# Optimization experiments

Measured on AMD Instinct MI355X. Metric: run time of the kernel, lower is better.

The kernel has to match this reference:

```python
import jax, jax.numpy as jnp
import numpy as np

N = 100_000      # nodes
E = 1_600_000    # edges (avg degree 16)
DIN = 128
DOUT = 128
NEG_SLOPE = 0.2  # DGL GATConv default negative_slope


def setup_inputs() -> dict:
    key = jax.random.key(0)
    k1, k2, k3, k4, k5, k6 = jax.random.split(key, 6)
    h = jax.random.normal(k1, (N, DIN), dtype=jnp.float32)
    src = jax.random.randint(k2, (E,), 0, N, dtype=jnp.int32)
    dst = jax.random.randint(k3, (E,), 0, N, dtype=jnp.int32)
    W = jax.random.normal(k4, (DIN, DOUT), dtype=jnp.float32) / np.sqrt(DIN).astype(np.float32)
    attn_l = jax.random.normal(k5, (DOUT,), dtype=jnp.float32) * 0.1
    attn_r = jax.random.normal(k6, (DOUT,), dtype=jnp.float32) * 0.1
    return {"h": h, "src": src, "dst": dst, "W": W, "attn_l": attn_l, "attn_r": attn_r}


def reference(h, src, dst, W, attn_l, attn_r):
    # Single-head DGL GATConv (bias=False, no feat/attn dropout, no activation).
    feat = h @ W                                   # [N, D] projected features
    el = feat @ attn_l                             # [N] source attention logits
    er = feat @ attn_r                             # [N] destination attention logits
    e = jax.nn.leaky_relu(el[src] + er[dst], NEG_SLOPE)   # [E] edge scores

    # Numerically stable edge softmax, grouped by destination node.
    m = jax.ops.segment_max(e, dst, num_segments=N)        # [N]
    m = jnp.where(jnp.isfinite(m), m, 0.0)                 # nodes with no in-edges
    ex = jnp.exp(e - m[dst])                               # [E]
    denom = jax.ops.segment_sum(ex, dst, num_segments=N)   # [N]
    alpha = ex / jnp.maximum(denom[dst], jnp.float32(1e-9))  # [E]

    # Weighted aggregation of source features into destination nodes.
    out = jax.ops.segment_sum(alpha[:, None] * feat[src], dst, num_segments=N)  # [N, D]
    return out
```

## Files before the change

### kernel.cpp

```cpp
#include <hip/hip_runtime.h>
#include <hip/hip_bf16.h>

#define N_NODES 100000
#define N_EDGES 1600000
#define D 128
#define NEG_SLOPE 0.2f

#define NBKT 782
#define CAPB 4096
#define BCHUNK 8192
#define BIN_BLOCKS 196
#define GEMM_BLOCKS 782
#define CAP 2816

typedef __attribute__((ext_vector_type(8))) short s8v;
typedef __attribute__((ext_vector_type(4))) float f4v;

static __device__ __forceinline__ unsigned short f2bf(float f) {
    __hip_bfloat16 b = __float2bfloat16(f);
    return *(unsigned short*)&b;
}

__global__ __launch_bounds__(256) void wcast(
    const float* __restrict__ W, const float* __restrict__ attn_l,
    const float* __restrict__ attn_r, unsigned short* __restrict__ Wt)
{
    __shared__ float Wl[128 * 132];
    __shared__ float all[128], arl[128];
    const int t = threadIdx.x;
    for (int i = 0; i < 64; ++i) {
        const int id = t + 256 * i;
        Wl[(id >> 7) * 132 + (id & 127)] = W[id];
    }
    if (t < 128) { all[t] = attn_l[t]; arl[t] = attn_r[t]; }
    __syncthreads();
    for (int i = 0; i < 64; ++i) {
        const int id = t + 256 * i;
        const int n = id >> 7, k = id & 127;
        Wt[n * 128 + k] = f2bf(Wl[k * 132 + n]);
    }
    if (t < 128) {
        float sl = 0.f, sr = 0.f;
        for (int n = 0; n < 128; ++n) {
            const float v = Wl[t * 132 + n];
            sl += v * all[n]; sr += v * arl[n];
        }
        Wt[128 * 128 + t] = f2bf(sl);
        Wt[129 * 128 + t] = f2bf(sr);
    }
}

__global__ __launch_bounds__(512) void gemm_bin(
    const float* __restrict__ h, const unsigned short* __restrict__ Wt,
    unsigned short* __restrict__ featb, float* __restrict__ el, float* __restrict__ er,
    const int* __restrict__ src, const int* __restrict__ dst,
    int* __restrict__ gwp, unsigned int* __restrict__ eb)
{
    __shared__ __align__(16) char smem[69632];
    const int t = threadIdx.x;

    if (blockIdx.x < BIN_BLOCKS) {
        int* cnt_l            = (int*)smem;
        int* tmp              = (int*)(smem + 3128);
        int* lbase            = (int*)(smem + 7224);
        int* gbase            = (int*)(smem + 10356);
        unsigned int* slocal  = (unsigned int*)(smem + 13484);
        unsigned short* sbkt  = (unsigned short*)(smem + 46252);

        const int base = (int)blockIdx.x * BCHUNK;
        const int nloc = min(BCHUNK, N_EDGES - base);

        for (int i = t; i < NBKT; i += 512) cnt_l[i] = 0;
        __syncthreads();

        unsigned int ent[16];
        unsigned short bk[16];
#pragma unroll
        for (int j = 0; j < 16; ++j) {
            const int i = t + 512 * j;
            if (i < nloc) {
                const int s = src[base + i];
                const int d = dst[base + i];
                bk[j]  = (unsigned short)(d >> 7);
                ent[j] = (unsigned int)s | ((unsigned int)(d & 127) << 17);
                atomicAdd(&cnt_l[bk[j]], 1);
            } else bk[j] = 0xffff;
        }
        __syncthreads();

        tmp[t]       = (t < NBKT) ? cnt_l[t] : 0;
        tmp[t + 512] = (t + 512 < NBKT) ? cnt_l[t + 512] : 0;
        __syncthreads();
        for (int o = 1; o < 1024; o <<= 1) {
            const int a  = (t >= o) ? tmp[t - o] : 0;
            const int b2 = (t + 512 >= o) ? tmp[t + 512 - o] : 0;
            __syncthreads();
            tmp[t] += a; tmp[t + 512] += b2;
            __syncthreads();
        }
        for (int i = t; i < NBKT; i += 512) lbase[i] = (i == 0) ? 0 : tmp[i - 1];
        if (t == 0) lbase[NBKT] = tmp[NBKT - 1];
        __syncthreads();

        for (int b = t; b < NBKT; b += 512) {
            const int c = lbase[b + 1] - lbase[b];
            if (c) gbase[b] = b * CAPB + atomicAdd(&gwp[b], c);
            cnt_l[b] = 0;
        }
        __syncthreads();

#pragma unroll
        for (int j = 0; j < 16; ++j) {
            if (bk[j] != 0xffff) {
                const int p = lbase[bk[j]] + atomicAdd(&cnt_l[bk[j]], 1);
                slocal[p] = ent[j];
                sbkt[p]   = bk[j];
            }
        }
        __syncthreads();

        for (int i = t; i < nloc; i += 512) {
            const int b = sbkt[i];
            eb[gbase[b] + (i - lbase[b])] = slocal[i];
        }
    } else {
        unsigned short* Asmem = (unsigned short*)smem;
        unsigned short* Bsmem = (unsigned short*)(smem + 32768);

        const int w    = t >> 6;
        const int lane = t & 63;
        const int g4   = lane >> 4;
        const int cl   = lane & 15;
        const int row0 = ((int)blockIdx.x - BIN_BLOCKS) * 128;

#pragma unroll
        for (int i = 0; i < 4; ++i) {
            const int ch = t + 512 * i;
            const int r = ch >> 4, c = ch & 15;
            const int srow = min(row0 + r, N_NODES - 1);
            const float4 a = *(const float4*)&h[srow * D + c * 8];
            const float4 b = *(const float4*)&h[srow * D + c * 8 + 4];
            s8v v;
            v[0] = (short)f2bf(a.x); v[1] = (short)f2bf(a.y);
            v[2] = (short)f2bf(a.z); v[3] = (short)f2bf(a.w);
            v[4] = (short)f2bf(b.x); v[5] = (short)f2bf(b.y);
            v[6] = (short)f2bf(b.z); v[7] = (short)f2bf(b.w);
            *(s8v*)&Asmem[r * 128 + ((c ^ (r & 15)) << 3)] = v;
        }
        for (int ch = t; ch < 2080; ch += 512) {
            const int n = ch >> 4, c = ch & 15;
            *(s8v*)&Bsmem[n * 128 + ((c ^ (n & 15)) << 3)] =
                *(const s8v*)&Wt[n * 128 + c * 8];
        }
        __syncthreads();

        f4v acc[9] = {};
#pragma unroll
        for (int ks = 0; ks < 4; ++ks) {
            const int c = ks * 4 + g4;
            s8v bfr[9];
#pragma unroll
            for (int nt = 0; nt < 9; ++nt) {
                const int n = nt * 16 + cl;
                bfr[nt] = *(const s8v*)&Bsmem[n * 128 + ((c ^ cl) << 3)];
            }
            const int r = w * 16 + cl;
            const s8v af = *(const s8v*)&Asmem[r * 128 + ((c ^ cl) << 3)];
#pragma unroll
            for (int nt = 0; nt < 9; ++nt)
                acc[nt] = __builtin_amdgcn_mfma_f32_16x16x32_bf16(
                    af, bfr[nt], acc[nt], 0, 0, 0);
        }

        unsigned short* ftile = Asmem;
#pragma unroll
        for (int nt = 0; nt < 8; ++nt) {
            const int ch = 2 * nt + (cl >> 3);
#pragma unroll
            for (int reg = 0; reg < 4; ++reg) {
                const int r = w * 16 + 4 * g4 + reg;
                ftile[r * 128 + ((ch ^ (r & 15)) << 3) + (cl & 7)] =
                    f2bf(acc[nt][reg]);
            }
        }
        if (cl < 2) {
            float* dstp = (cl == 0) ? el : er;
#pragma unroll
            for (int reg = 0; reg < 4; ++reg) {
                const int rg = row0 + w * 16 + 4 * g4 + reg;
                if (rg < N_NODES) dstp[rg] = acc[8][reg];
            }
        }
        __syncthreads();
#pragma unroll
        for (int i = 0; i < 4; ++i) {
            const int ch = t + 512 * i;
            const int r = ch >> 4, c = ch & 15;
            if (row0 + r < N_NODES)
                *(s8v*)&featb[(row0 + r) * 128 + c * 8] =
                    *(const s8v*)&ftile[r * 128 + ((c ^ (r & 15)) << 3)];
        }
    }
}

__global__ __launch_bounds__(512) void aggregate(
    const int* __restrict__ gwp, const unsigned int* __restrict__ eb,
    const float* __restrict__ el, const float* __restrict__ er,
    const uint2* __restrict__ featb2, float* __restrict__ out)
{
    __shared__ __align__(8) uint2 sw[CAP];
    __shared__ int off_l[129];
    __shared__ int cnt_l[128];
    __shared__ float nsum[128];
    __shared__ float er_l[128];

    const int t = threadIdx.x;
    const int b = blockIdx.x;
    const int ne   = gwp[b];
    const int gbeg = b * CAPB;
    const int node0 = b << 7;
    const int w    = t >> 6;
    const int lane = t & 63;
    const int ll   = lane & 31;
    const int half = lane >> 5;

    if (t < 128) {
        const int nd = node0 + t;
        er_l[t] = (nd < N_NODES) ? er[nd] : 0.f;
        cnt_l[t] = 0;
        nsum[t] = 0.f;
    }
    __syncthreads();

    if (ne <= CAP) {
        unsigned int ent[6];
#pragma unroll
        for (int j = 0; j < 6; ++j) {
            const int i = t + 512 * j;
            if (i < ne) {
                ent[j] = eb[gbeg + i];
                atomicAdd(&cnt_l[(ent[j] >> 17) & 127], 1);
            }
        }
        __syncthreads();
        if (w == 0) {
            const int a  = cnt_l[2 * lane];
            const int b2 = cnt_l[2 * lane + 1];
            int inc = a + b2;
#pragma unroll
            for (int o = 1; o < 64; o <<= 1) {
                const int u = __shfl_up(inc, o, 64);
                if (lane >= o) inc += u;
            }
            const int excl = inc - (a + b2);
            off_l[2 * lane]     = excl;
            off_l[2 * lane + 1] = excl + a;
            if (lane == 63) off_l[128] = inc;
            cnt_l[2 * lane] = 0; cnt_l[2 * lane + 1] = 0;
        }
        __syncthreads();
#pragma unroll
        for (int j = 0; j < 6; ++j) {
            const int i = t + 512 * j;
            if (i < ne) {
                const unsigned int e = ent[j];
                const int dl = (e >> 17) & 127;
                const int sj = (int)(e & 0x1FFFFu);
                float sc = el[sj] + er_l[dl];
                sc = (sc > 0.f) ? sc : NEG_SLOPE * sc;
                const float ex = __expf(sc);
                const int p = off_l[dl] + atomicAdd(&cnt_l[dl], 1);
                sw[p] = make_uint2(e, __float_as_uint(ex));
                atomicAdd(&nsum[dl], ex);
            }
        }
        __syncthreads();

        for (int dl = w; dl < 128; dl += 8) {
            const int node = node0 + dl;
            if (node >= N_NODES) break;
            const int beg = off_l[dl];
            const int n   = off_l[dl + 1] - beg;
            float4 acc = make_float4(0.f, 0.f, 0.f, 0.f);
            const int iters = (n + 1) >> 1;
            for (int tt = 0; tt < iters; ++tt) {
                const int idx = 2 * tt + half;
                const uint2 p = sw[beg + min(idx, n - 1)];
                const float wj = (idx < n) ? __uint_as_float(p.y) : 0.f;
                const int  sjj = (int)(p.x & 0x1FFFFu);
                const uint2 fb = featb2[sjj * 32 + ll];
                acc.x += wj * __uint_as_float(fb.x << 16);
                acc.y += wj * __uint_as_float(fb.x & 0xffff0000u);
                acc.z += wj * __uint_as_float(fb.y << 16);
                acc.w += wj * __uint_as_float(fb.y & 0xffff0000u);
            }
            acc.x += __shfl_xor(acc.x, 32, 64);
            acc.y += __shfl_xor(acc.y, 32, 64);
            acc.z += __shfl_xor(acc.z, 32, 64);
            acc.w += __shfl_xor(acc.w, 32, 64);
            const float rs = 1.f / fmaxf(nsum[dl], 1e-9f);
            if (lane < 32)
                *(float4*)&out[node * D + ll * 4] =
                    make_float4(acc.x * rs, acc.y * rs, acc.z * rs, acc.w * rs);
        }
    } else {
        for (int dl = w; dl < 128; dl += 8) {
            const int node = node0 + dl;
            if (node >= N_NODES) break;
            float4 acc = make_float4(0.f, 0.f, 0.f, 0.f);
            float ssum = 0.f;
            for (int ch = 0; ch < ne; ch += 64) {
                const int nn = min(64, ne - ch);
                float ex = 0.f; int sj = 0;
                if (lane < nn) {
                    const unsigned int e = eb[gbeg + ch + lane];
                    if ((int)((e >> 17) & 127) == dl) {
                        sj = (int)(e & 0x1FFFFu);
                        float sc = el[sj] + er_l[dl];
                        sc = (sc > 0.f) ? sc : NEG_SLOPE * sc;
                        ex = __expf(sc);
                    }
                }
                ssum += ex;
                const int iters = (nn + 1) >> 1;
                for (int tt = 0; tt < iters; ++tt) {
                    const int idx = 2 * tt + half;
                    const float wj = __shfl(ex, idx, 64);
                    const int  sjj = __shfl(sj, idx, 64);
                    if (wj > 0.f) {
                        const uint2 fb = featb2[sjj * 32 + ll];
                        acc.x += wj * __uint_as_float(fb.x << 16);
                        acc.y += wj * __uint_as_float(fb.x & 0xffff0000u);
                        acc.z += wj * __uint_as_float(fb.y << 16);
                        acc.w += wj * __uint_as_float(fb.y & 0xffff0000u);
                    }
                }
            }
#pragma unroll
            for (int o = 1; o < 64; o <<= 1) ssum += __shfl_xor(ssum, o, 64);
            acc.x += __shfl_xor(acc.x, 32, 64);
            acc.y += __shfl_xor(acc.y, 32, 64);
            acc.z += __shfl_xor(acc.z, 32, 64);
            acc.w += __shfl_xor(acc.w, 32, 64);
            const float rs = 1.f / fmaxf(ssum, 1e-9f);
            if (lane < 32)
                *(float4*)&out[node * D + ll * 4] =
                    make_float4(acc.x * rs, acc.y * rs, acc.z * rs, acc.w * rs);
        }
    }
}

extern "C" void kernel_launch(void* const* d_in, const int* in_sizes, int n_in,
                              void* d_out, int out_size, void* d_ws, size_t ws_size,
                              hipStream_t stream)
{
    const float* h      = (const float*)d_in[0];
    const int*   src    = (const int*)  d_in[1];
    const int*   dst    = (const int*)  d_in[2];
    const float* W      = (const float*)d_in[3];
    const float* attn_l = (const float*)d_in[4];
    const float* attn_r = (const float*)d_in[5];
    float* out = (float*)d_out;

    char* ws = (char*)d_ws;
    unsigned short* featb = (unsigned short*)ws; ws += (size_t)N_NODES * D * 2;
    unsigned short* Wt    = (unsigned short*)ws; ws += (size_t)130 * 128 * 2;
    ws = (char*)(((size_t)ws + 15) & ~(size_t)15);
    float* el  = (float*)ws; ws += (size_t)N_NODES * sizeof(float);
    float* er  = (float*)ws; ws += (size_t)N_NODES * sizeof(float);
    int*   gwp = (int*)ws;   ws += (size_t)NBKT * sizeof(int);
    ws = (char*)(((size_t)ws + 15) & ~(size_t)15);
    unsigned int* eb = (unsigned int*)ws; ws += (size_t)NBKT * CAPB * sizeof(unsigned int);

    hipMemsetAsync(gwp, 0, (size_t)NBKT * sizeof(int), stream);

    wcast<<<1, 256, 0, stream>>>(W, attn_l, attn_r, Wt);
    gemm_bin<<<BIN_BLOCKS + GEMM_BLOCKS, 512, 0, stream>>>(
        h, Wt, featb, el, er, src, dst, gwp, eb);
    aggregate<<<NBKT, 512, 0, stream>>>(gwp, eb, el, er, (const uint2*)featb, out);
}
```

Measured before the change: 206.2 us.

## Halve destination bucket size to 64 nodes and parallelize weight cast

Destination buckets shrink from 128 to 64 nodes, which doubles the number of aggregate blocks (1563) and binning blocks while halving the per-block edge chunk, capacity and shared memory. The binning prefix scan is extended to cover up to 2048 buckets. The weight transpose/cast kernel is split across 17 blocks that read W directly from global memory instead of staging it through shared memory in a single block. The aim is more parallelism and better occupancy on the GPU, at the cost of more global atomics on bucket counters and a longer scan.

```diff
diff --git a/kernel.cpp b/kernel.cpp
--- a/kernel.cpp
+++ b/kernel.cpp
@@ -6,12 +6,12 @@
 #define D 128
 #define NEG_SLOPE 0.2f
 
-#define NBKT 782
-#define CAPB 4096
-#define BCHUNK 8192
-#define BIN_BLOCKS 196
+#define NBKT 1563
+#define CAPB 2048
+#define BCHUNK 4096
+#define BIN_BLOCKS 391
 #define GEMM_BLOCKS 782
-#define CAP 2816
+#define CAP 1536
 
 typedef __attribute__((ext_vector_type(8))) short s8v;
 typedef __attribute__((ext_vector_type(4))) float f4v;
@@ -19,34 +19,40 @@
 static __device__ __forceinline__ unsigned short f2bf(float f) {
     __hip_bfloat16 b = __float2bfloat16(f);
     return *(unsigned short*)&b;
+}
+static __device__ __forceinline__ float bflo(unsigned int u) {
+    return __uint_as_float(u << 16);
+}
+static __device__ __forceinline__ float bfhi(unsigned int u) {
+    return __uint_as_float(u & 0xffff0000u);
 }
 
 __global__ __launch_bounds__(256) void wcast(
     const float* __restrict__ W, const float* __restrict__ attn_l,
     const float* __restrict__ attn_r, unsigned short* __restrict__ Wt)
 {
-    __shared__ float Wl[128 * 132];
-    __shared__ float all[128], arl[128];
     const int t = threadIdx.x;
-    for (int i = 0; i < 64; ++i) {
-        const int id = t + 256 * i;
-        Wl[(id >> 7) * 132 + (id & 127)] = W[id];
-    }
-    if (t < 128) { all[t] = attn_l[t]; arl[t] = attn_r[t]; }
-    __syncthreads();
-    for (int i = 0; i < 64; ++i) {
-        const int id = t + 256 * i;
-        const int n = id >> 7, k = id & 127;
-        Wt[n * 128 + k] = f2bf(Wl[k * 132 + n]);
-    }
-    if (t < 128) {
-        float sl = 0.f, sr = 0.f;
-        for (int n = 0; n < 128; ++n) {
-            const float v = Wl[t * 132 + n];
-            sl += v * all[n]; sr += v * arl[n];
-        }
-        Wt[128 * 128 + t] = f2bf(sl);
-        Wt[129 * 128 + t] = f2bf(sr);
+    if (blockIdx.x < 16) {
+        const int n0 = blockIdx.x * 8;
+#pragma unroll
+        for (int i = 0; i < 4; ++i) {
+            const int id = t + 256 * i;
+            const int n = n0 + (id >> 7), k = id & 127;
+            Wt[n * 128 + k] = f2bf(W[k * 128 + n]);
+        }
+    } else {
+        __shared__ float all[128], arl[128];
+        if (t < 128) { all[t] = attn_l[t]; arl[t] = attn_r[t]; }
+        __syncthreads();
+        if (t < 128) {
+            float sl = 0.f, sr = 0.f;
+            for (int n = 0; n < 128; ++n) {
+                const float v = W[t * 128 + n];
+                sl += v * all[n]; sr += v * arl[n];
+            }
+            Wt[128 * 128 + t] = f2bf(sl);
+            Wt[129 * 128 + t] = f2bf(sr);
+        }
     }
 }
 
@@ -61,11 +67,11 @@
 
     if (blockIdx.x < BIN_BLOCKS) {
         int* cnt_l            = (int*)smem;
-        int* tmp              = (int*)(smem + 3128);
-        int* lbase            = (int*)(smem + 7224);
-        int* gbase            = (int*)(smem + 10356);
-        unsigned int* slocal  = (unsigned int*)(smem + 13484);
-        unsigned short* sbkt  = (unsigned short*)(smem + 46252);
+        int* lbase            = (int*)(smem + 6256);
+        int* gbase            = (int*)(smem + 12528);
+        int* tmp              = (int*)(smem + 18784);
+        unsigned int* slocal  = (unsigned int*)(smem + 26976);
+        unsigned short* sbkt  = (unsigned short*)(smem + 43360);
 
         const int base = (int)blockIdx.x * BCHUNK;
         const int nloc = min(BCHUNK, N_EDGES - base);
@@ -73,29 +79,37 @@
         for (int i = t; i < NBKT; i += 512) cnt_l[i] = 0;
         __syncthreads();
 
-        unsigned int ent[16];
-        unsigned short bk[16];
-#pragma unroll
-        for (int j = 0; j < 16; ++j) {
+        unsigned int ent[8];
+        unsigned short bk[8];
+#pragma unroll
+        for (int j = 0; j < 8; ++j) {
             const int i = t + 512 * j;
             if (i < nloc) {
                 const int s = src[base + i];
                 const int d = dst[base + i];
-                bk[j]  = (unsigned short)(d >> 7);
-                ent[j] = (unsigned int)s | ((unsigned int)(d & 127) << 17);
+                bk[j]  = (unsigned short)(d >> 6);
+                ent[j] = (unsigned int)s | ((unsigned int)(d & 63) << 17);
                 atomicAdd(&cnt_l[bk[j]], 1);
             } else bk[j] = 0xffff;
         }
         __syncthreads();
 
-        tmp[t]       = (t < NBKT) ? cnt_l[t] : 0;
-        tmp[t + 512] = (t + 512 < NBKT) ? cnt_l[t + 512] : 0;
-        __syncthreads();
-        for (int o = 1; o < 1024; o <<= 1) {
-            const int a  = (t >= o) ? tmp[t - o] : 0;
-            const int b2 = (t + 512 >= o) ? tmp[t + 512 - o] : 0;
+#pragma unroll
+        for (int j = 0; j < 4; ++j) {
+            const int i = t + 512 * j;
+            tmp[i] = (i < NBKT) ? cnt_l[i] : 0;
+        }
+        __syncthreads();
+        for (int o = 1; o < 2048; o <<= 1) {
+            int a[4];
+#pragma unroll
+            for (int j = 0; j < 4; ++j) {
+                const int i = t + 512 * j;
+                a[j] = (i >= o) ? tmp[i - o] : 0;
+            }
             __syncthreads();
-            tmp[t] += a; tmp[t + 512] += b2;
+#pragma unroll
+            for (int j = 0; j < 4; ++j) tmp[t + 512 * j] += a[j];
             __syncthreads();
         }
         for (int i = t; i < NBKT; i += 512) lbase[i] = (i == 0) ? 0 : tmp[i - 1];
@@ -110,7 +124,7 @@
         __syncthreads();
 
 #pragma unroll
-        for (int j = 0; j < 16; ++j) {
+        for (int j = 0; j < 8; ++j) {
             if (bk[j] != 0xffff) {
                 const int p = lbase[bk[j]] + atomicAdd(&cnt_l[bk[j]], 1);
                 slocal[p] = ent[j];
@@ -209,22 +223,22 @@
     const uint2* __restrict__ featb2, float* __restrict__ out)
 {
     __shared__ __align__(8) uint2 sw[CAP];
-    __shared__ int off_l[129];
-    __shared__ int cnt_l[128];
-    __shared__ float nsum[128];
-    __shared__ float er_l[128];
+    __shared__ int off_l[65];
+    __shared__ int cnt_l[64];
+    __shared__ float nsum[64];
+    __shared__ float er_l[64];
 
     const int t = threadIdx.x;
     const int b = blockIdx.x;
     const int ne   = gwp[b];
     const int gbeg = b * CAPB;
-    const int node0 = b << 7;
+    const int node0 = b << 6;
     const int w    = t >> 6;
     const int lane = t & 63;
     const int ll   = lane & 31;
     const int half = lane >> 5;
 
-    if (t < 128) {
+    if (t < 64) {
         const int nd = node0 + t;
         er_l[t] = (nd < N_NODES) ? er[nd] : 0.f;
         cnt_l[t] = 0;
@@ -233,38 +247,35 @@
     __syncthreads();
 
     if (ne <= CAP) {
-        unsigned int ent[6];
-#pragma unroll
-        for (int j = 0; j < 6; ++j) {
+        unsigned int ent[3];
+#pragma unroll
+        for (int j = 0; j < 3; ++j) {
             const int i = t + 512 * j;
             if (i < ne) {
                 ent[j] = eb[gbeg + i];
-                atomicAdd(&cnt_l[(ent[j] >> 17) & 127], 1);
+                atomicAdd(&cnt_l[(ent[j] >> 17) & 63], 1);
             }
         }
         __syncthreads();
         if (w == 0) {
-            const int a  = cnt_l[2 * lane];
-            const int b2 = cnt_l[2 * lane + 1];
-            int inc = a + b2;
+            const int v = cnt_l[lane];
+            int inc = v;
 #pragma unroll
             for (int o = 1; o < 64; o <<= 1) {
                 const int u = __shfl_up(inc, o, 64);
                 if (lane >= o) inc += u;
             }
-            const int excl = inc - (a + b2);
-            off_l[2 * lane]     = excl;
-            off_l[2 * lane + 1] = excl + a;
-            if (lane == 63) off_l[128] = inc;
-            cnt_l[2 * lane] = 0; cnt_l[2 * lane + 1] = 0;
-        }
-        __syncthreads();
-#pragma unroll
-        for (int j = 0; j < 6; ++j) {
+            off_l[lane] = inc - v;
+            if (lane == 63) off_l[64] = inc;
+            cnt_l[lane] = 0;
+        }
+        __syncthreads();
+#pragma unroll
+        for (int j = 0; j < 3; ++j) {
             const int i = t + 512 * j;
             if (i < ne) {
                 const unsigned int e = ent[j];
-                const int dl = (e >> 17) & 127;
+                const int dl = (e >> 17) & 63;
                 const int sj = (int)(e & 0x1FFFFu);
                 float sc = el[sj] + er_l[dl];
                 sc = (sc > 0.f) ? sc : NEG_SLOPE * sc;
@@ -276,7 +287,7 @@
         }
         __syncthreads();
 
-        for (int dl = w; dl < 128; dl += 8) {
+        for (int dl = w; dl < 64; dl += 8) {
             const int node = node0 + dl;
             if (node >= N_NODES) break;
             const int beg = off_l[dl];
@@ -289,10 +300,8 @@
                 const float wj = (idx < n) ? __uint_as_float(p.y) : 0.f;
                 const int  sjj = (int)(p.x & 0x1FFFFu);
                 const uint2 fb = featb2[sjj * 32 + ll];
-                acc.x += wj * __uint_as_float(fb.x << 16);
-                acc.y += wj * __uint_as_float(fb.x & 0xffff0000u);
-                acc.z += wj * __uint_as_float(fb.y << 16);
-                acc.w += wj * __uint_as_float(fb.y & 0xffff0000u);
+                acc.x += wj * bflo(fb.x); acc.y += wj * bfhi(fb.x);
+                acc.z += wj * bflo(fb.y); acc.w += wj * bfhi(fb.y);
             }
             acc.x += __shfl_xor(acc.x, 32, 64);
             acc.y += __shfl_xor(acc.y, 32, 64);
@@ -304,7 +313,7 @@
                     make_float4(acc.x * rs, acc.y * rs, acc.z * rs, acc.w * rs);
         }
     } else {
-        for (int dl = w; dl < 128; dl += 8) {
+        for (int dl = w; dl < 64; dl += 8) {
             const int node = node0 + dl;
             if (node >= N_NODES) break;
             float4 acc = make_float4(0.f, 0.f, 0.f, 0.f);
@@ -314,7 +323,7 @@
                 float ex = 0.f; int sj = 0;
                 if (lane < nn) {
                     const unsigned int e = eb[gbeg + ch + lane];
-                    if ((int)((e >> 17) & 127) == dl) {
+                    if ((int)((e >> 17) & 63) == dl) {
                         sj = (int)(e & 0x1FFFFu);
                         float sc = el[sj] + er_l[dl];
                         sc = (sc > 0.f) ? sc : NEG_SLOPE * sc;
@@ -329,10 +338,8 @@
                     const int  sjj = __shfl(sj, idx, 64);
                     if (wj > 0.f) {
                         const uint2 fb = featb2[sjj * 32 + ll];
-                        acc.x += wj * __uint_as_float(fb.x << 16);
-                        acc.y += wj * __uint_as_float(fb.x & 0xffff0000u);
-                        acc.z += wj * __uint_as_float(fb.y << 16);
-                        acc.w += wj * __uint_as_float(fb.y & 0xffff0000u);
+                        acc.x += wj * bflo(fb.x); acc.y += wj * bfhi(fb.x);
+                        acc.z += wj * bflo(fb.y); acc.w += wj * bfhi(fb.y);
                     }
                 }
             }
@@ -374,7 +381,7 @@
 
     hipMemsetAsync(gwp, 0, (size_t)NBKT * sizeof(int), stream);
 
-    wcast<<<1, 256, 0, stream>>>(W, attn_l, attn_r, Wt);
+    wcast<<<17, 256, 0, stream>>>(W, attn_l, attn_r, Wt);
     gemm_bin<<<BIN_BLOCKS + GEMM_BLOCKS, 512, 0, stream>>>(
         h, Wt, featb, el, er, src, dst, gwp, eb);
     aggregate<<<NBKT, 512, 0, stream>>>(gwp, eb, el, er, (const uint2*)featb, out);
```

New measurement: 210.9 us. 1.02x slower.
